# Optimization experiments

Measured on AMD Instinct MI355X. Metric: run time of the kernel, lower is better.

Reference implementation:

```python
import jax, jax.numpy as jnp
import numpy as np

N_NODES = 100000
N_EDGES = 1600000
N_GRAPHS = 4096
IN_DIM, HID, OUT_DIM = 128, 128, 64
BN_EPS = 1e-5


def gcn_conv(x, W, b, src, dst):
    """PyG GCNConv: symmetric norm with self-loops. x:[N,Fin] -> [N,Fout]."""
    h = x @ W  # [N, Fout]
    ones = jnp.ones((src.shape[0],), dtype=h.dtype)
    deg = jax.ops.segment_sum(ones, dst, num_segments=N_NODES) + 1.0  # +1 for self-loop
    dinv = jax.lax.rsqrt(deg)  # deg >= 1, safe
    norm = dinv[src] * dinv[dst]  # [E]
    msg = h[src] * norm[:, None]  # [E, Fout] gather + scale
    agg = jax.ops.segment_sum(msg, dst, num_segments=N_NODES)
    agg = agg + h * (dinv * dinv)[:, None]  # self-loop term, norm = dinv_i^2
    return agg + b


def batchnorm(x, gamma, beta):
    mu = jnp.mean(x, axis=0)
    var = jnp.mean(jnp.square(x - mu), axis=0)  # biased var, torch BN training mode
    return (x - mu) * jax.lax.rsqrt(var + BN_EPS) * gamma + beta


def setup_inputs() -> dict:
    key = jax.random.key(0)
    ks = jax.random.split(key, 12)
    x = jax.random.normal(ks[0], (N_NODES, IN_DIM), dtype=jnp.float32)
    edge_index = jax.random.randint(ks[1], (2, N_EDGES), 0, N_NODES, dtype=jnp.int64)
    batch = jnp.sort(jax.random.randint(ks[2], (N_NODES,), 0, N_GRAPHS, dtype=jnp.int64))
    def lin(k, fi, fo):
        s = 1.0 / np.sqrt(fi)
        return jax.random.uniform(k, (fi, fo), jnp.float32, -s, s)
    return {
        "x": x, "edge_index": edge_index, "batch": batch,
        "W1": lin(ks[3], IN_DIM, HID), "b1": jnp.zeros((HID,), jnp.float32),
        "g1": jnp.ones((HID,), jnp.float32), "be1": jnp.zeros((HID,), jnp.float32),
        "W2": lin(ks[4], HID, HID), "b2": jnp.zeros((HID,), jnp.float32),
        "g2": jnp.ones((HID,), jnp.float32), "be2": jnp.zeros((HID,), jnp.float32),
        "W3": lin(ks[5], HID, HID), "b3": jnp.zeros((HID,), jnp.float32),
        "g3": jnp.ones((HID,), jnp.float32), "be3": jnp.zeros((HID,), jnp.float32),
        "fcW": lin(ks[6], HID, OUT_DIM),
        "fcb": jax.random.uniform(ks[7], (OUT_DIM,), jnp.float32, -1/np.sqrt(HID), 1/np.sqrt(HID)),
    }


def reference(x, edge_index, batch, W1, b1, g1, be1, W2, b2, g2, be2, W3, b3, g3, be3, fcW, fcb):
    src, dst = edge_index[0], edge_index[1]
    h = jax.nn.relu(batchnorm(gcn_conv(x, W1, b1, src, dst), g1, be1))
    h = jax.nn.relu(batchnorm(gcn_conv(h, W2, b2, src, dst), g2, be2))
    h = jax.nn.relu(batchnorm(gcn_conv(h, W3, b3, src, dst), g3, be3))
    # global mean pool over graphs
    sums = jax.ops.segment_sum(h, batch, num_segments=N_GRAPHS)  # [G, HID]
    cnt = jax.ops.segment_sum(jnp.ones((N_NODES,), h.dtype), batch, num_segments=N_GRAPHS)
    pooled = sums / jnp.maximum(cnt, 1.0)[:, None]
    return pooled @ fcW + fcb
```

## Files before the change

### kernel.cpp

```cpp
#include <hip/hip_runtime.h>

#define NN 100000
#define NE 1600000
#define NG 4096
#define HID 128
#define ODIM 64
#define BN_EPS 1e-5f
#define NBUK 782
#define BPAD 896
#define NZROW 256
#define CHUNK 16384
#define PREP_HIST 256
#define PREP_GOFF 17
#define PREP_W 192

typedef unsigned int u32;
typedef unsigned short u16;
typedef short short8 __attribute__((ext_vector_type(8)));
typedef float f32x4 __attribute__((ext_vector_type(4)));

__device__ inline u32 pack_bf16(float a, float b) {
  u32 ua = __float_as_uint(a), ub = __float_as_uint(b);
  ua += 0x7fffu + ((ua >> 16) & 1u);
  ub += 0x7fffu + ((ub >> 16) & 1u);
  return (ua >> 16) | (ub & 0xffff0000u);
}
__device__ inline u16 bf16_of(float v) {
  u32 ua = __float_as_uint(v);
  ua += 0x7fffu + ((ua >> 16) & 1u);
  return (u16)(ua >> 16);
}
__device__ inline float bf_lo(u32 u) { return __uint_as_float(u << 16); }
__device__ inline float bf_hi(u32 u) { return __uint_as_float(u & 0xffff0000u); }

__global__ __launch_bounds__(256) void k_prep(const int* __restrict__ ei, int* __restrict__ bcnt,
                                              const int* __restrict__ batch, int* __restrict__ goff,
                                              const float* __restrict__ W1, const float* __restrict__ W2,
                                              const float* __restrict__ W3, u16* __restrict__ Wt1,
                                              u16* __restrict__ Wt2, u16* __restrict__ Wt3) {
  __shared__ int h[NBUK];
  int b = blockIdx.x, t = threadIdx.x;
  if (b < PREP_HIST) {
    for (int i = t; i < NBUK; i += 256) h[i] = 0;
    __syncthreads();
    const int stride = PREP_HIST * 256;
    for (int e = b * 256 + t; e < NE; e += stride)
      atomicAdd(&h[ei[NE + e] >> 7], 1);
    __syncthreads();
    for (int i = t; i < NBUK; i += 256)
      if (h[i]) atomicAdd(&bcnt[i], h[i]);
  } else if (b < PREP_HIST + PREP_GOFF) {
    int g = (b - PREP_HIST) * 256 + t;
    if (g <= NG) {
      int lo = 0, hi = NN;
      while (lo < hi) { int mid = (lo + hi) >> 1; if (batch[mid] < g) lo = mid + 1; else hi = mid; }
      goff[g] = lo;
    }
  } else {
    int idx = (b - PREP_HIST - PREP_GOFF) * 256 + t;
    int mat = idx >> 14;
    int rem = idx & 16383;
    int n = rem >> 7, k = rem & 127;
    const float* W = (mat == 0) ? W1 : (mat == 1) ? W2 : W3;
    u16* Wt = (mat == 0) ? Wt1 : (mat == 1) ? Wt2 : Wt3;
    Wt[(n << 7) + k] = bf16_of(W[(k << 7) + n]);
  }
}

__global__ __launch_bounds__(1024) void k_bscan(const int* __restrict__ bcnt, int* __restrict__ bboff,
                                                int* __restrict__ bcur) {
  __shared__ int ls[1024];
  int t = threadIdx.x;
  ls[t] = (t < NBUK) ? bcnt[t] : 0;
  __syncthreads();
  for (int d = 1; d < 1024; d <<= 1) {
    int v = 0;
    if (t >= d) v = ls[t - d];
    __syncthreads();
    ls[t] += v;
    __syncthreads();
  }
  if (t < NBUK) {
    int ex = (t == 0) ? 0 : ls[t - 1];
    bboff[t] = ex;
    bcur[t] = ex;
  }
  if (t == 0) bboff[NBUK] = NE;
}

__global__ __launch_bounds__(1024) void k_bscatter(const int* __restrict__ ei, int* __restrict__ bcur,
                                                   u32* __restrict__ ebuf) {
  __shared__ int cnt[NBUK], rnk[NBUK], base[NBUK];
  int t = threadIdx.x;
  int e0 = blockIdx.x * CHUNK;
  for (int i = t; i < NBUK; i += 1024) { cnt[i] = 0; rnk[i] = 0; }
  __syncthreads();
  for (int i = t; i < CHUNK; i += 1024) {
    int e = e0 + i;
    if (e < NE) atomicAdd(&cnt[ei[NE + e] >> 7], 1);
  }
  __syncthreads();
  for (int i = t; i < NBUK; i += 1024) {
    int c = cnt[i];
    base[i] = c ? atomicAdd(&bcur[i], c) : 0;
  }
  __syncthreads();
  for (int i = t; i < CHUNK; i += 1024) {
    int e = e0 + i;
    if (e < NE) {
      int s = ei[e], d = ei[NE + e];
      int b = d >> 7;
      int r = atomicAdd(&rnk[b], 1);
      ebuf[base[b] + r] = ((u32)(d & 127) << 17) | (u32)s;
    }
  }
}

__global__ __launch_bounds__(256) void k_csr(const u32* __restrict__ ebuf, const int* __restrict__ bboff,
                                             int* __restrict__ off, int* __restrict__ oend,
                                             float* __restrict__ dinv, u32* __restrict__ csrc) {
  __shared__ int cnt[128], scn[128], cur[128];
  int b = blockIdx.x, t = threadIdx.x;
  int n0 = b << 7;
  int ebeg = bboff[b], eend = bboff[b + 1];
  int pboff = ebeg + BPAD * b;
  if (t < 128) cnt[t] = 0;
  __syncthreads();
  for (int e = ebeg + t; e < eend; e += 256) atomicAdd(&cnt[ebuf[e] >> 17], 1);
  __syncthreads();
  int pc = 0;
  if (t < 128) { pc = (cnt[t] + 7) & ~7; scn[t] = pc; }
  __syncthreads();
  for (int d = 1; d < 128; d <<= 1) {
    int v = 0;
    if (t >= d && t < 128) v = scn[t - d];
    __syncthreads();
    if (t < 128) scn[t] += v;
    __syncthreads();
  }
  int nvalid = min(128, NN - n0);
  if (t < 128) {
    int ex = scn[t] - pc;
    cur[t] = ex;
    if (t < nvalid) {
      off[n0 + t] = pboff + ex;
      oend[n0 + t] = pboff + scn[t];
      dinv[n0 + t] = rsqrtf((float)cnt[t] + 1.0f);
    }
  }
  __syncthreads();
  for (int e = ebeg + t; e < eend; e += 256) {
    u32 p = ebuf[e];
    int d = p >> 17;
    int pos = pboff + atomicAdd(&cur[d], 1);
    csrc[pos] = (p & 0x1ffffu) << 8;
  }
  if (t < 128) {
    int ex = scn[t] - pc;
    for (int i = cnt[t]; i < pc; ++i)
      csrc[pboff + ex + i] = (u32)(NN + ((n0 + t + i) & (NZROW - 1))) << 8;
  }
}

__global__ __launch_bounds__(256) void k_gemm1(const float* __restrict__ A, const u16* __restrict__ Wt,
                                               const float* __restrict__ dinv, u16* __restrict__ H) {
  __shared__ u16 Bs[4][128][32];
  u16 (*Ct)[128] = (u16 (*)[128])&Bs[0][0][0];
  int t = threadIdx.x;
  int w = t >> 6, l = t & 63;
  int quad = l >> 4, lid = l & 15;
  int row0 = blockIdx.x * 128;

  {
    const uint4* src = (const uint4*)Wt;
#pragma unroll
    for (int rep = 0; rep < 8; ++rep) {
      int i = rep * 256 + t;
      int n = i >> 4, j = i & 15;
      *(uint4*)&Bs[j >> 2][n][(j & 3) << 3] = src[i];
    }
  }

  f32x4 acc[2][8];
#pragma unroll
  for (int mt = 0; mt < 2; ++mt)
#pragma unroll
    for (int nt = 0; nt < 8; ++nt) acc[mt][nt] = (f32x4){0.f, 0.f, 0.f, 0.f};

  int ra0 = row0 + (w << 5) + lid;
  int ra1 = ra0 + 16;
  bool ok0 = ra0 < NN, ok1 = ra1 < NN;
  int cb = quad << 3;
  __syncthreads();

#pragma unroll
  for (int ks = 0; ks < 4; ++ks) {
    int k0 = ks << 5;
    float4 f0 = {0, 0, 0, 0}, f1 = {0, 0, 0, 0}, f2 = {0, 0, 0, 0}, f3 = {0, 0, 0, 0};
    if (ok0) {
      const float4* ap = (const float4*)(A + (size_t)ra0 * HID + k0 + cb);
      f0 = ap[0]; f1 = ap[1];
    }
    if (ok1) {
      const float4* ap = (const float4*)(A + (size_t)ra1 * HID + k0 + cb);
      f2 = ap[0]; f3 = ap[1];
    }
    uint4 ua, ub;
    ua.x = pack_bf16(f0.x, f0.y); ua.y = pack_bf16(f0.z, f0.w);
    ua.z = pack_bf16(f1.x, f1.y); ua.w = pack_bf16(f1.z, f1.w);
    ub.x = pack_bf16(f2.x, f2.y); ub.y = pack_bf16(f2.z, f2.w);
    ub.z = pack_bf16(f3.x, f3.y); ub.w = pack_bf16(f3.z, f3.w);
    short8 a0, a1;
    *(uint4*)&a0 = ua;
    *(uint4*)&a1 = ub;
#pragma unroll
    for (int nt = 0; nt < 8; ++nt) {
      short8 b = *(const short8*)&Bs[ks][(nt << 4) + lid][cb];
      acc[0][nt] = __builtin_amdgcn_mfma_f32_16x16x32_bf16(a0, b, acc[0][nt], 0, 0, 0);
      acc[1][nt] = __builtin_amdgcn_mfma_f32_16x16x32_bf16(a1, b, acc[1][nt], 0, 0, 0);
    }
  }
  __syncthreads();

  int valid = min(128, NN - row0);
#pragma unroll
  for (int mt = 0; mt < 2; ++mt) {
#pragma unroll
    for (int r = 0; r < 4; ++r) {
      int rl = (w << 5) + (mt << 4) + (quad << 2) + r;
      float dv = (rl < valid) ? dinv[row0 + rl] : 0.f;
#pragma unroll
      for (int nt = 0; nt < 8; ++nt) {
        Ct[rl][(nt << 4) + lid] = bf16_of(acc[mt][nt][r] * dv);
      }
    }
  }
  __syncthreads();
  u16* Hb = H + (size_t)row0 * HID;
  int tot = valid << 4;
  for (int idx = t; idx < tot; idx += 256) {
    ((uint4*)Hb)[idx] = ((const uint4*)Ct)[idx];
  }
}

__device__ inline u32 bn_pair(u32 v, float2 sc, float2 sh) {
  float a = fmaxf(fmaf(bf_lo(v), sc.x, sh.x), 0.f);
  float b = fmaxf(fmaf(bf_hi(v), sc.y, sh.y), 0.f);
  return pack_bf16(a, b);
}

__global__ __launch_bounds__(256) void k_gemm_b(const u16* __restrict__ A, const u16* __restrict__ Wt,
                                                const float* __restrict__ sums, const float* __restrict__ g,
                                                const float* __restrict__ be,
                                                const float* __restrict__ dinv, u16* __restrict__ H) {
  __shared__ u16 Bs[4][128][32];
  __shared__ float scsh[256];
  u16 (*Ct)[128] = (u16 (*)[128])&Bs[0][0][0];
  int t = threadIdx.x;
  int w = t >> 6, l = t & 63;
  int quad = l >> 4, lid = l & 15;
  int row0 = blockIdx.x * 128;

  if (t < 128) {
    const float invN = 1.0f / (float)NN;
    float mu = sums[t] * invN;
    float var = sums[HID + t] * invN - mu * mu;
    float sc = g[t] * rsqrtf(var + BN_EPS);
    scsh[t] = sc;
    scsh[128 + t] = be[t] - mu * sc;
  }
  {
    const uint4* src = (const uint4*)Wt;
#pragma unroll
    for (int rep = 0; rep < 8; ++rep) {
      int i = rep * 256 + t;
      int n = i >> 4, j = i & 15;
      *(uint4*)&Bs[j >> 2][n][(j & 3) << 3] = src[i];
    }
  }

  f32x4 acc[2][8];
#pragma unroll
  for (int mt = 0; mt < 2; ++mt)
#pragma unroll
    for (int nt = 0; nt < 8; ++nt) acc[mt][nt] = (f32x4){0.f, 0.f, 0.f, 0.f};

  int ra0 = row0 + (w << 5) + lid;
  int ra1 = ra0 + 16;
  bool ok0 = ra0 < NN, ok1 = ra1 < NN;
  int cb = quad << 3;
  __syncthreads();

#pragma unroll
  for (int ks = 0; ks < 4; ++ks) {
    int k0 = ks << 5;
    uint4 qa = {0, 0, 0, 0}, qb = {0, 0, 0, 0};
    if (ok0) qa = *(const uint4*)(A + (size_t)ra0 * HID + k0 + cb);
    if (ok1) qb = *(const uint4*)(A + (size_t)ra1 * HID + k0 + cb);
    const float2* scp = (const float2*)(scsh + k0 + cb);
    const float2* shp = (const float2*)(scsh + 128 + k0 + cb);
    float2 s0 = scp[0], s1 = scp[1], s2 = scp[2], s3 = scp[3];
    float2 h0 = shp[0], h1 = shp[1], h2 = shp[2], h3 = shp[3];
    qa.x = bn_pair(qa.x, s0, h0); qa.y = bn_pair(qa.y, s1, h1);
    qa.z = bn_pair(qa.z, s2, h2); qa.w = bn_pair(qa.w, s3, h3);
    qb.x = bn_pair(qb.x, s0, h0); qb.y = bn_pair(qb.y, s1, h1);
    qb.z = bn_pair(qb.z, s2, h2); qb.w = bn_pair(qb.w, s3, h3);
    short8 a0, a1;
    *(uint4*)&a0 = qa;
    *(uint4*)&a1 = qb;
#pragma unroll
    for (int nt = 0; nt < 8; ++nt) {
      short8 b = *(const short8*)&Bs[ks][(nt << 4) + lid][cb];
      acc[0][nt] = __builtin_amdgcn_mfma_f32_16x16x32_bf16(a0, b, acc[0][nt], 0, 0, 0);
      acc[1][nt] = __builtin_amdgcn_mfma_f32_16x16x32_bf16(a1, b, acc[1][nt], 0, 0, 0);
    }
  }
  __syncthreads();

  int valid = min(128, NN - row0);
#pragma unroll
  for (int mt = 0; mt < 2; ++mt) {
#pragma unroll
    for (int r = 0; r < 4; ++r) {
      int rl = (w << 5) + (mt << 4) + (quad << 2) + r;
      float dv = (rl < valid) ? dinv[row0 + rl] : 0.f;
#pragma unroll
      for (int nt = 0; nt < 8; ++nt) {
        Ct[rl][(nt << 4) + lid] = bf16_of(acc[mt][nt][r] * dv);
      }
    }
  }
  __syncthreads();
  u16* Hb = H + (size_t)row0 * HID;
  int tot = valid << 4;
  for (int idx = t; idx < tot; idx += 256) {
    ((uint4*)Hb)[idx] = ((const uint4*)Ct)[idx];
  }
}

__global__ __launch_bounds__(256) void k_agg(const u16* __restrict__ h2, const int* __restrict__ off,
                                             const int* __restrict__ oend, const u32* __restrict__ csrc,
                                             const float* __restrict__ dinv, u16* __restrict__ aggb) {
  int node = (int)((blockIdx.x * 256 + threadIdx.x) >> 6);
  int lane = threadIdx.x & 63;
  if (node >= NN) return;
  int half = lane >> 5;
  u32 lb8 = (u32)(lane & 31) << 3;
  const char* h2b = (const char*)h2;
  int beg = off[node], end = oend[node];
  float f0 = 0.f, f1 = 0.f, f2 = 0.f, f3 = 0.f;
  if (half == 0) {
    uint2 us = *(const uint2*)(h2b + (((size_t)node << 8) + lb8));
    f0 = bf_lo(us.x); f1 = bf_hi(us.x); f2 = bf_lo(us.y); f3 = bf_hi(us.y);
  }
  int e = beg;
  for (; e + 16 <= end; e += 16) {
    u32 s[8]; uint2 v[8];
#pragma unroll
    for (int i = 0; i < 8; ++i) s[i] = csrc[e + 2 * i + half];
#pragma unroll
    for (int i = 0; i < 8; ++i) v[i] = *(const uint2*)(h2b + ((size_t)s[i] + lb8));
#pragma unroll
    for (int i = 0; i < 8; ++i) {
      f0 += bf_lo(v[i].x); f1 += bf_hi(v[i].x);
      f2 += bf_lo(v[i].y); f3 += bf_hi(v[i].y);
    }
  }
  if (e < end) {
    u32 s[4]; uint2 v[4];
#pragma unroll
    for (int i = 0; i < 4; ++i) s[i] = csrc[e + 2 * i + half];
#pragma unroll
    for (int i = 0; i < 4; ++i) v[i] = *(const uint2*)(h2b + ((size_t)s[i] + lb8));
#pragma unroll
    for (int i = 0; i < 4; ++i) {
      f0 += bf_lo(v[i].x); f1 += bf_hi(v[i].x);
      f2 += bf_lo(v[i].y); f3 += bf_hi(v[i].y);
    }
  }
  f0 += __shfl_xor(f0, 32, 64);
  f1 += __shfl_xor(f1, 32, 64);
  f2 += __shfl_xor(f2, 32, 64);
  f3 += __shfl_xor(f3, 32, 64);
  if (half == 0) {
    float di = dinv[node];
    uint2 p;
    p.x = pack_bf16(f0 * di, f1 * di);
    p.y = pack_bf16(f2 * di, f3 * di);
    *(uint2*)((char*)aggb + (((size_t)node << 8) + lb8)) = p;
  }
}

__global__ __launch_bounds__(256) void k_bnstats(const u16* __restrict__ X, float* __restrict__ buf) {
  __shared__ float lsx[256], lssx[256], lsy[256], lssy[256];
  int t = threadIdx.x;
  int colp = t & 63, grp = t >> 6;
  int rbeg = blockIdx.x * 256, rend = min(rbeg + 256, NN);
  float sx = 0.f, ssx = 0.f, sy = 0.f, ssy = 0.f;
  for (int r = rbeg + grp; r < rend; r += 4) {
    u32 v = ((const u32*)(X + (size_t)r * HID))[colp];
    float a = bf_lo(v), b = bf_hi(v);
    sx += a; ssx = fmaf(a, a, ssx);
    sy += b; ssy = fmaf(b, b, ssy);
  }
  lsx[t] = sx; lssx[t] = ssx; lsy[t] = sy; lssy[t] = ssy;
  __syncthreads();
  if (t < 64) {
    sx = lsx[t] + lsx[t + 64] + lsx[t + 128] + lsx[t + 192];
    ssx = lssx[t] + lssx[t + 64] + lssx[t + 128] + lssx[t + 192];
    sy = lsy[t] + lsy[t + 64] + lsy[t + 128] + lsy[t + 192];
    ssy = lssy[t] + lssy[t + 64] + lssy[t + 128] + lssy[t + 192];
    atomicAdd(&buf[2 * colp], sx);
    atomicAdd(&buf[2 * colp + 1], sy);
    atomicAdd(&buf[HID + 2 * colp], ssx);
    atomicAdd(&buf[HID + 2 * colp + 1], ssy);
  }
}

__global__ __launch_bounds__(256) void k_poolfc(const u16* __restrict__ aggb, const float* __restrict__ sums,
                                                const float* __restrict__ g3, const float* __restrict__ be3,
                                                const int* __restrict__ goff, const float* __restrict__ fcW,
                                                const float* __restrict__ fcb, float* __restrict__ out) {
  __shared__ float ls[4][128];
  int t = threadIdx.x;
  int w = t >> 6, lane = t & 63;
  int gr = blockIdx.x * 4 + w;
  const float invN = 1.0f / (float)NN;
  int f0 = lane << 1, f1 = f0 + 1;
  float mu0 = sums[f0] * invN, mu1 = sums[f1] * invN;
  float v0 = sums[HID + f0] * invN - mu0 * mu0;
  float v1 = sums[HID + f1] * invN - mu1 * mu1;
  float sc0 = g3[f0] * rsqrtf(v0 + BN_EPS), sc1 = g3[f1] * rsqrtf(v1 + BN_EPS);
  float sh0 = be3[f0] - mu0 * sc0, sh1 = be3[f1] - mu1 * sc1;
  int beg = goff[gr], end = goff[gr + 1];
  float ax = 0.f, ay = 0.f;
  for (int r = beg; r < end; ++r) {
    u32 v = ((const u32*)(aggb + (size_t)r * HID))[lane];
    ax += fmaxf(fmaf(bf_lo(v), sc0, sh0), 0.f);
    ay += fmaxf(fmaf(bf_hi(v), sc1, sh1), 0.f);
  }
  float inv = 1.0f / fmaxf((float)(end - beg), 1.0f);
  ls[w][f0] = ax * inv;
  ls[w][f1] = ay * inv;
  __syncthreads();
  float acc = fcb[lane];
#pragma unroll 8
  for (int k = 0; k < HID; ++k) acc = fmaf(ls[w][k], fcW[(size_t)k * ODIM + lane], acc);
  out[(size_t)gr * ODIM + lane] = acc;
}

extern "C" void kernel_launch(void* const* d_in, const int* in_sizes, int n_in,
                              void* d_out, int out_size, void* d_ws, size_t ws_size,
                              hipStream_t stream) {
  const float* x     = (const float*)d_in[0];
  const int*   ei    = (const int*)d_in[1];
  const int*   batch = (const int*)d_in[2];
  const float* W1    = (const float*)d_in[3];
  const float* g1    = (const float*)d_in[5];
  const float* be1   = (const float*)d_in[6];
  const float* W2    = (const float*)d_in[7];
  const float* g2    = (const float*)d_in[9];
  const float* be2   = (const float*)d_in[10];
  const float* W3    = (const float*)d_in[11];
  const float* g3    = (const float*)d_in[13];
  const float* be3   = (const float*)d_in[14];
  const float* fcW   = (const float*)d_in[15];
  const float* fcb   = (const float*)d_in[16];
  float* out = (float*)d_out;

  char* p = (char*)d_ws;
  auto alloc = [&](size_t bytes) { char* r = p; p += (bytes + 255) & ~(size_t)255; return r; };
  int*   bcnt   = (int*)alloc((size_t)NBUK * 4);
  float* bnb    = (float*)alloc(3 * 256 * 4);
  size_t zbytes = (size_t)(p - (char*)d_ws);
  int*   bboff  = (int*)alloc((size_t)(NBUK + 1) * 4);
  int*   bcur   = (int*)alloc((size_t)NBUK * 4);
  int*   off    = (int*)alloc((size_t)NN * 4);
  int*   oend   = (int*)alloc((size_t)NN * 4);
  float* dinv   = (float*)alloc((size_t)NN * 4);
  u32*   ebuf   = (u32*)alloc((size_t)NE * 4);
  u32*   csrc   = (u32*)alloc(((size_t)NE + (size_t)BPAD * NBUK) * 4);
  int*   goff   = (int*)alloc((size_t)(NG + 1) * 4);
  u16*   Wt1    = (u16*)alloc((size_t)HID * HID * 2);
  u16*   Wt2    = (u16*)alloc((size_t)HID * HID * 2);
  u16*   Wt3    = (u16*)alloc((size_t)HID * HID * 2);
  u16*   h2     = (u16*)alloc((size_t)(NN + NZROW) * HID * 2);
  u16*   aggb   = (u16*)alloc((size_t)NN * HID * 2);

  hipMemsetAsync(d_ws, 0, zbytes, stream);
  hipMemsetAsync(h2 + (size_t)NN * HID, 0, (size_t)NZROW * HID * 2, stream);

  const int NB = (NN + 255) / 256;
  const int GB = (NN + 127) / 128;
  const int AGB = NN / 4;
  const int SB = (NE + CHUNK - 1) / CHUNK;

  k_prep<<<PREP_HIST + PREP_GOFF + PREP_W, 256, 0, stream>>>(ei, bcnt, batch, goff, W1, W2, W3, Wt1, Wt2, Wt3);
  k_bscan<<<1, 1024, 0, stream>>>(bcnt, bboff, bcur);
  k_bscatter<<<SB, 1024, 0, stream>>>(ei, bcur, ebuf);
  k_csr<<<NBUK, 256, 0, stream>>>(ebuf, bboff, off, oend, dinv, csrc);

  k_gemm1<<<GB, 256, 0, stream>>>(x, Wt1, dinv, h2);
  k_agg<<<AGB, 256, 0, stream>>>(h2, off, oend, csrc, dinv, aggb);
  k_bnstats<<<NB, 256, 0, stream>>>(aggb, bnb);
  k_gemm_b<<<GB, 256, 0, stream>>>(aggb, Wt2, bnb, g1, be1, dinv, h2);
  k_agg<<<AGB, 256, 0, stream>>>(h2, off, oend, csrc, dinv, aggb);
  k_bnstats<<<NB, 256, 0, stream>>>(aggb, bnb + 256);
  k_gemm_b<<<GB, 256, 0, stream>>>(aggb, Wt3, bnb + 256, g2, be2, dinv, h2);
  k_agg<<<AGB, 256, 0, stream>>>(h2, off, oend, csrc, dinv, aggb);
  k_bnstats<<<NB, 256, 0, stream>>>(aggb, bnb + 512);
  k_poolfc<<<NG / 4, 256, 0, stream>>>(aggb, bnb + 512, g3, be3, goff, fcW, fcb, out);
}
```

Baseline: 522.1 us.

## Split aggregation feature dimension across two block halves

The aggregation kernel now launches twice as many blocks, and each block handles one 64-feature half of every node's 128 bf16 features. Each lane gathers 4 bytes instead of 8 per source edge. The goal is more parallelism and more gathers in flight to hide gather latency. In exchange, the CSR offsets and source indices are read twice and each gather request is narrower, which may reduce memory efficiency.

```diff
diff --git a/kernel.cpp b/kernel.cpp
--- a/kernel.cpp
+++ b/kernel.cpp
@@ -13,6 +13,7 @@
 #define PREP_HIST 256
 #define PREP_GOFF 17
 #define PREP_W 192
+#define AGB (NN / 4)
 
 typedef unsigned int u32;
 typedef unsigned short u16;
@@ -341,53 +342,45 @@
 __global__ __launch_bounds__(256) void k_agg(const u16* __restrict__ h2, const int* __restrict__ off,
                                              const int* __restrict__ oend, const u32* __restrict__ csrc,
                                              const float* __restrict__ dinv, u16* __restrict__ aggb) {
-  int node = (int)((blockIdx.x * 256 + threadIdx.x) >> 6);
+  int gid = blockIdx.x;
+  u32 fh = 0;
+  if (gid >= AGB) { fh = 1; gid -= AGB; }
+  int node = (int)((gid * 256 + threadIdx.x) >> 6);
   int lane = threadIdx.x & 63;
   if (node >= NN) return;
   int half = lane >> 5;
-  u32 lb8 = (u32)(lane & 31) << 3;
+  u32 lb4 = ((u32)(lane & 31) << 2) | (fh << 7);
   const char* h2b = (const char*)h2;
   int beg = off[node], end = oend[node];
-  float f0 = 0.f, f1 = 0.f, f2 = 0.f, f3 = 0.f;
+  float f0 = 0.f, f1 = 0.f;
   if (half == 0) {
-    uint2 us = *(const uint2*)(h2b + (((size_t)node << 8) + lb8));
-    f0 = bf_lo(us.x); f1 = bf_hi(us.x); f2 = bf_lo(us.y); f3 = bf_hi(us.y);
+    u32 us = *(const u32*)(h2b + (((size_t)node << 8) + lb4));
+    f0 = bf_lo(us); f1 = bf_hi(us);
   }
   int e = beg;
   for (; e + 16 <= end; e += 16) {
-    u32 s[8]; uint2 v[8];
+    u32 s[8], v[8];
 #pragma unroll
     for (int i = 0; i < 8; ++i) s[i] = csrc[e + 2 * i + half];
 #pragma unroll
-    for (int i = 0; i < 8; ++i) v[i] = *(const uint2*)(h2b + ((size_t)s[i] + lb8));
-#pragma unroll
-    for (int i = 0; i < 8; ++i) {
-      f0 += bf_lo(v[i].x); f1 += bf_hi(v[i].x);
-      f2 += bf_lo(v[i].y); f3 += bf_hi(v[i].y);
-    }
+    for (int i = 0; i < 8; ++i) v[i] = *(const u32*)(h2b + ((size_t)s[i] + lb4));
+#pragma unroll
+    for (int i = 0; i < 8; ++i) { f0 += bf_lo(v[i]); f1 += bf_hi(v[i]); }
   }
   if (e < end) {
-    u32 s[4]; uint2 v[4];
+    u32 s[4], v[4];
 #pragma unroll
     for (int i = 0; i < 4; ++i) s[i] = csrc[e + 2 * i + half];
 #pragma unroll
-    for (int i = 0; i < 4; ++i) v[i] = *(const uint2*)(h2b + ((size_t)s[i] + lb8));
-#pragma unroll
-    for (int i = 0; i < 4; ++i) {
-      f0 += bf_lo(v[i].x); f1 += bf_hi(v[i].x);
-      f2 += bf_lo(v[i].y); f3 += bf_hi(v[i].y);
-    }
+    for (int i = 0; i < 4; ++i) v[i] = *(const u32*)(h2b + ((size_t)s[i] + lb4));
+#pragma unroll
+    for (int i = 0; i < 4; ++i) { f0 += bf_lo(v[i]); f1 += bf_hi(v[i]); }
   }
   f0 += __shfl_xor(f0, 32, 64);
   f1 += __shfl_xor(f1, 32, 64);
-  f2 += __shfl_xor(f2, 32, 64);
-  f3 += __shfl_xor(f3, 32, 64);
   if (half == 0) {
     float di = dinv[node];
-    uint2 p;
-    p.x = pack_bf16(f0 * di, f1 * di);
-    p.y = pack_bf16(f2 * di, f3 * di);
-    *(uint2*)((char*)aggb + (((size_t)node << 8) + lb8)) = p;
+    *(u32*)((char*)aggb + (((size_t)node << 8) + lb4)) = pack_bf16(f0 * di, f1 * di);
   }
 }
 
@@ -492,7 +485,6 @@
 
   const int NB = (NN + 255) / 256;
   const int GB = (NN + 127) / 128;
-  const int AGB = NN / 4;
   const int SB = (NE + CHUNK - 1) / CHUNK;
 
   k_prep<<<PREP_HIST + PREP_GOFF + PREP_W, 256, 0, stream>>>(ei, bcnt, batch, goff, W1, W2, W3, Wt1, Wt2, Wt3);
@@ -501,13 +493,13 @@
   k_csr<<<NBUK, 256, 0, stream>>>(ebuf, bboff, off, oend, dinv, csrc);
 
   k_gemm1<<<GB, 256, 0, stream>>>(x, Wt1, dinv, h2);
-  k_agg<<<AGB, 256, 0, stream>>>(h2, off, oend, csrc, dinv, aggb);
+  k_agg<<<2 * AGB, 256, 0, stream>>>(h2, off, oend, csrc, dinv, aggb);
   k_bnstats<<<NB, 256, 0, stream>>>(aggb, bnb);
   k_gemm_b<<<GB, 256, 0, stream>>>(aggb, Wt2, bnb, g1, be1, dinv, h2);
-  k_agg<<<AGB, 256, 0, stream>>>(h2, off, oend, csrc, dinv, aggb);
+  k_agg<<<2 * AGB, 256, 0, stream>>>(h2, off, oend, csrc, dinv, aggb);
   k_bnstats<<<NB, 256, 0, stream>>>(aggb, bnb + 256);
   k_gemm_b<<<GB, 256, 0, stream>>>(aggb, Wt3, bnb + 256, g2, be2, dinv, h2);
-  k_agg<<<AGB, 256, 0, stream>>>(h2, off, oend, csrc, dinv, aggb);
+  k_agg<<<2 * AGB, 256, 0, stream>>>(h2, off, oend, csrc, dinv, aggb);
   k_bnstats<<<NB, 256, 0, stream>>>(aggb, bnb + 512);
   k_poolfc<<<NG / 4, 256, 0, stream>>>(aggb, bnb + 512, g3, be3, goff, fcW, fcb, out);
 }
```

New measurement: 546.8 us. 1.05x slower.

## Fuse batchnorm statistics accumulation into the aggregation kernel

Applied to the files above, without the earlier changes.

Removes the separate k_bnstats pass. Each aggregation block now reduces its four nodes' per-feature sums and sums of squares in shared memory and atomically adds them to the BN stats buffer. This saves one full read of the aggregated activations per layer and one launch per layer. In exchange, it issues far more global float atomics (256 per 4-node block, tens of thousands of blocks) onto the same 256 addresses, which risks heavy atomic contention. It also adds a block-wide barrier to the latency-bound gather kernel.

```diff
diff --git a/kernel.cpp b/kernel.cpp
--- a/kernel.cpp
+++ b/kernel.cpp
@@ -340,10 +340,13 @@
 
 __global__ __launch_bounds__(256) void k_agg(const u16* __restrict__ h2, const int* __restrict__ off,
                                              const int* __restrict__ oend, const u32* __restrict__ csrc,
-                                             const float* __restrict__ dinv, u16* __restrict__ aggb) {
-  int node = (int)((blockIdx.x * 256 + threadIdx.x) >> 6);
-  int lane = threadIdx.x & 63;
-  if (node >= NN) return;
+                                             const float* __restrict__ dinv, u16* __restrict__ aggb,
+                                             float* __restrict__ bnbO) {
+  __shared__ float red[4][128], rsq[4][128];
+  int t = threadIdx.x;
+  int wv = t >> 6;
+  int node = (int)((blockIdx.x * 256 + t) >> 6);
+  int lane = t & 63;
   int half = lane >> 5;
   u32 lb8 = (u32)(lane & 31) << 3;
   const char* h2b = (const char*)h2;
@@ -382,38 +385,25 @@
   f1 += __shfl_xor(f1, 32, 64);
   f2 += __shfl_xor(f2, 32, 64);
   f3 += __shfl_xor(f3, 32, 64);
+  float di = dinv[node];
+  float d0 = f0 * di, d1 = f1 * di, d2 = f2 * di, d3 = f3 * di;
+  int fb = (lane & 31) << 2;
   if (half == 0) {
-    float di = dinv[node];
     uint2 p;
-    p.x = pack_bf16(f0 * di, f1 * di);
-    p.y = pack_bf16(f2 * di, f3 * di);
+    p.x = pack_bf16(d0, d1);
+    p.y = pack_bf16(d2, d3);
     *(uint2*)((char*)aggb + (((size_t)node << 8) + lb8)) = p;
-  }
-}
-
-__global__ __launch_bounds__(256) void k_bnstats(const u16* __restrict__ X, float* __restrict__ buf) {
-  __shared__ float lsx[256], lssx[256], lsy[256], lssy[256];
-  int t = threadIdx.x;
-  int colp = t & 63, grp = t >> 6;
-  int rbeg = blockIdx.x * 256, rend = min(rbeg + 256, NN);
-  float sx = 0.f, ssx = 0.f, sy = 0.f, ssy = 0.f;
-  for (int r = rbeg + grp; r < rend; r += 4) {
-    u32 v = ((const u32*)(X + (size_t)r * HID))[colp];
-    float a = bf_lo(v), b = bf_hi(v);
-    sx += a; ssx = fmaf(a, a, ssx);
-    sy += b; ssy = fmaf(b, b, ssy);
-  }
-  lsx[t] = sx; lssx[t] = ssx; lsy[t] = sy; lssy[t] = ssy;
-  __syncthreads();
-  if (t < 64) {
-    sx = lsx[t] + lsx[t + 64] + lsx[t + 128] + lsx[t + 192];
-    ssx = lssx[t] + lssx[t + 64] + lssx[t + 128] + lssx[t + 192];
-    sy = lsy[t] + lsy[t + 64] + lsy[t + 128] + lsy[t + 192];
-    ssy = lssy[t] + lssy[t + 64] + lssy[t + 128] + lssy[t + 192];
-    atomicAdd(&buf[2 * colp], sx);
-    atomicAdd(&buf[2 * colp + 1], sy);
-    atomicAdd(&buf[HID + 2 * colp], ssx);
-    atomicAdd(&buf[HID + 2 * colp + 1], ssy);
+    red[wv][fb] = d0; red[wv][fb + 1] = d1; red[wv][fb + 2] = d2; red[wv][fb + 3] = d3;
+  } else {
+    rsq[wv][fb] = d0 * d0; rsq[wv][fb + 1] = d1 * d1;
+    rsq[wv][fb + 2] = d2 * d2; rsq[wv][fb + 3] = d3 * d3;
+  }
+  __syncthreads();
+  if (t < 128) {
+    float s = red[0][t] + red[1][t] + red[2][t] + red[3][t];
+    float q = rsq[0][t] + rsq[1][t] + rsq[2][t] + rsq[3][t];
+    atomicAdd(&bnbO[t], s);
+    atomicAdd(&bnbO[HID + t], q);
   }
 }
 
@@ -490,7 +480,6 @@
   hipMemsetAsync(d_ws, 0, zbytes, stream);
   hipMemsetAsync(h2 + (size_t)NN * HID, 0, (size_t)NZROW * HID * 2, stream);
 
-  const int NB = (NN + 255) / 256;
   const int GB = (NN + 127) / 128;
   const int AGB = NN / 4;
   const int SB = (NE + CHUNK - 1) / CHUNK;
@@ -501,13 +490,10 @@
   k_csr<<<NBUK, 256, 0, stream>>>(ebuf, bboff, off, oend, dinv, csrc);
 
   k_gemm1<<<GB, 256, 0, stream>>>(x, Wt1, dinv, h2);
-  k_agg<<<AGB, 256, 0, stream>>>(h2, off, oend, csrc, dinv, aggb);
-  k_bnstats<<<NB, 256, 0, stream>>>(aggb, bnb);
+  k_agg<<<AGB, 256, 0, stream>>>(h2, off, oend, csrc, dinv, aggb, bnb);
   k_gemm_b<<<GB, 256, 0, stream>>>(aggb, Wt2, bnb, g1, be1, dinv, h2);
-  k_agg<<<AGB, 256, 0, stream>>>(h2, off, oend, csrc, dinv, aggb);
-  k_bnstats<<<NB, 256, 0, stream>>>(aggb, bnb + 256);
+  k_agg<<<AGB, 256, 0, stream>>>(h2, off, oend, csrc, dinv, aggb, bnb + 256);
   k_gemm_b<<<GB, 256, 0, stream>>>(aggb, Wt3, bnb + 256, g2, be2, dinv, h2);
-  k_agg<<<AGB, 256, 0, stream>>>(h2, off, oend, csrc, dinv, aggb);
-  k_bnstats<<<NB, 256, 0, stream>>>(aggb, bnb + 512);
+  k_agg<<<AGB, 256, 0, stream>>>(h2, off, oend, csrc, dinv, aggb, bnb + 512);
   k_poolfc<<<NG / 4, 256, 0, stream>>>(aggb, bnb + 512, g3, be3, goff, fcW, fcb, out);
 }
```

Measured after the change: 2.066 ms. 296% more time.
